# Optimization experiments

Measured on AMD Instinct MI355X. Metric: run time of the kernel, lower is better.

## Reference

```python
import jax, jax.numpy as jnp
import numpy as np

# Static multi-scale feature-map shapes (H, W) per level; sum(H*W) = 21760 = Len_in.
SPATIAL_SHAPES = ((128, 128), (64, 64), (32, 32), (16, 16))
N_HEADS, N_LEVELS, N_POINTS = 8, 4, 4


def _sample_level(v, loc, H, W):
    """Bilinear grid-sample, align_corners=False, zero padding.
    v:   (N, M, H*W, D) per-level value
    loc: (N, Lq, M, P, 2) sampling locations in [0,1] (x, y order)
    returns (N, Lq, M, P, D)
    """
    N, M, _, D = v.shape
    _, Lq, _, P, _ = loc.shape
    g = 2.0 * loc - 1.0                              # grid in [-1, 1]
    x = ((g[..., 0] + 1.0) * W - 1.0) * 0.5          # (N, Lq, M, P) pixel coords
    y = ((g[..., 1] + 1.0) * H - 1.0) * 0.5
    x0 = jnp.floor(x)
    y0 = jnp.floor(y)
    out = jnp.zeros((N, M, Lq * P, D), dtype=v.dtype)
    for dy in (0, 1):
        for dx in (0, 1):
            xi = x0 + dx
            yi = y0 + dy
            w = (1.0 - jnp.abs(x - xi)) * (1.0 - jnp.abs(y - yi))
            valid = (xi >= 0) & (xi <= W - 1) & (yi >= 0) & (yi <= H - 1)
            w = jnp.where(valid, w, 0.0)             # zero padding outside
            xc = jnp.clip(xi, 0, W - 1).astype(jnp.int32)
            yc = jnp.clip(yi, 0, H - 1).astype(jnp.int32)
            idx = yc * W + xc                        # (N, Lq, M, P)
            idx = jnp.transpose(idx, (0, 2, 1, 3)).reshape(N, M, Lq * P)
            gathered = jnp.take_along_axis(v, idx[..., None], axis=2)  # (N, M, Lq*P, D)
            wt = jnp.transpose(w, (0, 2, 1, 3)).reshape(N, M, Lq * P, 1)
            out = out + gathered * wt
    out = out.reshape(N, M, Lq, P, D)
    return jnp.transpose(out, (0, 2, 1, 3, 4))       # (N, Lq, M, P, D)


def _ms_deform_attn_core(value, sampling_locations, attention_weights):
    # value: (N, Len_in, M, D); locs: (N, Lq, M, L, P, 2); attn: (N, Lq, M, L, P)
    N, _, M, D = value.shape
    Lq = sampling_locations.shape[1]
    acc = jnp.zeros((N, Lq, M, D), dtype=value.dtype)
    start = 0
    for lid, (H, W) in enumerate(SPATIAL_SHAPES):
        v_l = value[:, start:start + H * W]                    # (N, H*W, M, D)
        v_l = jnp.transpose(v_l, (0, 2, 1, 3))                 # (N, M, H*W, D)
        samp = _sample_level(v_l, sampling_locations[:, :, :, lid], H, W)
        acc = acc + jnp.einsum('nqmpd,nqmp->nqmd', samp, attention_weights[:, :, :, lid])
        start += H * W
    return acc.reshape(N, Lq, M * D)


def setup_inputs() -> dict:
    key = jax.random.key(0)
    ks = jax.random.split(key, 12)
    N, Lq, C = 2, 21760, 256
    L, P, M = N_LEVELS, N_POINTS, N_HEADS
    s = 0.05  # keep logits / offsets in a sane range
    return {
        'query': jax.random.normal(ks[0], (N, Lq, C), jnp.float32),
        'reference_points': jax.random.uniform(ks[1], (N, Lq, L, 2), jnp.float32),
        'input_flatten': jax.random.normal(ks[2], (N, Lq, C), jnp.float32),
        'W_off': jax.random.normal(ks[3], (C, M * L * P * 2), jnp.float32) * s,
        'b_off': jax.random.normal(ks[4], (M * L * P * 2,), jnp.float32) * s,
        'W_attn': jax.random.normal(ks[5], (C, M * L * P), jnp.float32) * s,
        'b_attn': jax.random.normal(ks[6], (M * L * P,), jnp.float32) * s,
        'W_val': jax.random.normal(ks[7], (C, C), jnp.float32) * s,
        'b_val': jax.random.normal(ks[8], (C,), jnp.float32) * s,
        'W_out': jax.random.normal(ks[9], (C, C), jnp.float32) * s,
        'b_out': jax.random.normal(ks[10], (C,), jnp.float32) * s,
    }


def reference(query, reference_points, input_flatten, W_off, b_off,
              W_attn, b_attn, W_val, b_val, W_out, b_out):
    N, Lq, C = query.shape
    M, L, P = N_HEADS, N_LEVELS, N_POINTS
    D = C // M
    value = (input_flatten @ W_val + b_val).reshape(N, -1, M, D)
    offsets = (query @ W_off + b_off).reshape(N, Lq, M, L, P, 2)
    attn = (query @ W_attn + b_attn).reshape(N, Lq, M, L * P)
    attn = jax.nn.softmax(attn, axis=-1).reshape(N, Lq, M, L, P)
    # offset normalizer is (W_l, H_l) per level
    norm = jnp.array([[w, h] for (h, w) in SPATIAL_SHAPES], dtype=query.dtype)  # (L, 2)
    loc = (reference_points[:, :, None, :, None, :]
           + offsets / norm[None, None, None, :, None, :])   # (N, Lq, M, L, P, 2)
    out = _ms_deform_attn_core(value, loc, attn)
    return out @ W_out + b_out
```

## Files before the change

### kernel.cpp

```cpp
#include <hip/hip_runtime.h>

#define LQ     21760
#define NBATCH 2
#define MROWS  (NBATCH * LQ)
#define QB     (MROWS / 8)

typedef __attribute__((ext_vector_type(8))) short bf16x8;
typedef __attribute__((ext_vector_type(4))) float f32x4;

__device__ __forceinline__ unsigned short f2bf(float f) {
    unsigned u = __builtin_bit_cast(unsigned, f);
    return (unsigned short)((u + 0x7fffu + ((u >> 16) & 1u)) >> 16);
}
__device__ __forceinline__ float bf2f(unsigned short h) {
    return __builtin_bit_cast(float, (unsigned)h << 16);
}
__device__ __forceinline__ float f16lo(unsigned u) {
    return (float)__builtin_bit_cast(_Float16, (unsigned short)(u & 0xffffu));
}
__device__ __forceinline__ float f16hi(unsigned u) {
    return (float)__builtin_bit_cast(_Float16, (unsigned short)(u >> 16));
}

template <int CTRL>
__device__ __forceinline__ float fdpp(float v) {
    int r = __builtin_amdgcn_update_dpp(
        0, __builtin_bit_cast(int, v), CTRL, 0xf, 0xf, false);
    return __builtin_bit_cast(float, r);
}

__global__ __launch_bounds__(256) void cvt_wall(
    const float* __restrict__ Wv, const float* __restrict__ Wo,
    const float* __restrict__ Wa, const float* __restrict__ Wu,
    short* __restrict__ Wtv, short* __restrict__ Wcat, short* __restrict__ Wtu)
{
    int idx = blockIdx.x * 256 + threadIdx.x;
    if (idx < 65536) {
        int nn = idx >> 8, k = idx & 255;
        Wtv[idx] = (short)f2bf(Wv[k * 256 + nn]);
    } else if (idx < 131072) {
        int j = idx - 65536; int nn = j >> 8, k = j & 255;
        Wcat[j] = (short)f2bf(Wo[k * 256 + nn]);
    } else if (idx < 163840) {
        int j = idx - 131072; int nn = j >> 8, k = j & 255;
        Wcat[65536 + j] = (short)f2bf(Wa[k * 128 + nn]);
    } else if (idx < 229376) {
        int j = idx - 163840; int nn = j >> 8, k = j & 255;
        Wtu[j] = (short)f2bf(Wu[k * 256 + nn]);
    }
}

template <int AF32, int OMODE>
__global__ __launch_bounds__(256) void gemm_mfma(
    const void* __restrict__ Aptr,
    const short* __restrict__ Bt,
    const float* __restrict__ bias,
    const float* __restrict__ bias2,
    void* __restrict__ Cout,
    void* __restrict__ Cout2,
    int N)
{
    __shared__ short Al[128 * 64];
    __shared__ short Bl[128 * 64];

    const int tid  = threadIdx.x;
    const int lane = tid & 63, wid = tid >> 6;
    const int wr = wid >> 1, wc = wid & 1;
    const int bx = blockIdx.x, by = blockIdx.y;

    const long arow0 = (long)by * 128;
    const int  brow0 = bx * 128;

    const short* Abf = (const short*)Aptr;
    const float* Af  = (const float*)Aptr;

    f32x4 acc[4][4];
#pragma unroll
    for (int i = 0; i < 4; ++i)
#pragma unroll
        for (int j = 0; j < 4; ++j) acc[i][j] = (f32x4)0.f;

    bf16x8 ra[4], rb[4];
    float4 raf[4][2];

#pragma unroll
    for (int i = 0; i < 4; ++i) {
        int id = tid + i * 256, r = id >> 3, c = id & 7;
        if (AF32) {
            raf[i][0] = *(const float4*)(Af + (arow0 + r) * 256 + c * 8);
            raf[i][1] = *(const float4*)(Af + (arow0 + r) * 256 + c * 8 + 4);
        } else {
            ra[i] = *(const bf16x8*)(Abf + (arow0 + r) * 256 + c * 8);
        }
        rb[i] = *(const bf16x8*)(Bt + (long)(brow0 + r) * 256 + c * 8);
    }

    for (int step = 0; step < 4; ++step) {
#pragma unroll
        for (int i = 0; i < 4; ++i) {
            int id = tid + i * 256, r = id >> 3, c = id & 7;
            bf16x8 av;
            if (AF32) {
                unsigned q0, q1, q2, q3;
                asm("v_cvt_pk_bf16_f32 %0, %1, %2" : "=v"(q0) : "v"(raf[i][0].x), "v"(raf[i][0].y));
                asm("v_cvt_pk_bf16_f32 %0, %1, %2" : "=v"(q1) : "v"(raf[i][0].z), "v"(raf[i][0].w));
                asm("v_cvt_pk_bf16_f32 %0, %1, %2" : "=v"(q2) : "v"(raf[i][1].x), "v"(raf[i][1].y));
                asm("v_cvt_pk_bf16_f32 %0, %1, %2" : "=v"(q3) : "v"(raf[i][1].z), "v"(raf[i][1].w));
                uint4 u = make_uint4(q0, q1, q2, q3);
                av = __builtin_bit_cast(bf16x8, u);
            } else {
                av = ra[i];
            }
            *(bf16x8*)(Al + r * 64 + ((c ^ (r & 7)) * 8)) = av;
            *(bf16x8*)(Bl + r * 64 + ((c ^ (r & 7)) * 8)) = rb[i];
        }
        __syncthreads();
        if (step < 3) {
            const int k0 = (step + 1) * 64;
#pragma unroll
            for (int i = 0; i < 4; ++i) {
                int id = tid + i * 256, r = id >> 3, c = id & 7;
                if (AF32) {
                    raf[i][0] = *(const float4*)(Af + (arow0 + r) * 256 + k0 + c * 8);
                    raf[i][1] = *(const float4*)(Af + (arow0 + r) * 256 + k0 + c * 8 + 4);
                } else {
                    ra[i] = *(const bf16x8*)(Abf + (arow0 + r) * 256 + k0 + c * 8);
                }
                rb[i] = *(const bf16x8*)(Bt + (long)(brow0 + r) * 256 + k0 + c * 8);
            }
        }
#pragma unroll
        for (int kk = 0; kk < 2; ++kk) {
            const int g = lane >> 4;
            const int chunk = kk * 4 + g;
            bf16x8 af[4], bg[4];
#pragma unroll
            for (int mi = 0; mi < 4; ++mi) {
                int r = wr * 64 + mi * 16 + (lane & 15);
                af[mi] = *(const bf16x8*)(Al + r * 64 + ((chunk ^ (r & 7)) * 8));
            }
#pragma unroll
            for (int ni = 0; ni < 4; ++ni) {
                int r = wc * 64 + ni * 16 + (lane & 15);
                bg[ni] = *(const bf16x8*)(Bl + r * 64 + ((chunk ^ (r & 7)) * 8));
            }
#pragma unroll
            for (int mi = 0; mi < 4; ++mi)
#pragma unroll
                for (int ni = 0; ni < 4; ++ni)
                    acc[mi][ni] = __builtin_amdgcn_mfma_f32_16x16x32_bf16(
                        af[mi], bg[ni], acc[mi][ni], 0, 0, 0);
        }
        __syncthreads();
    }

#pragma unroll
    for (int mi = 0; mi < 4; ++mi) {
#pragma unroll
        for (int ni = 0; ni < 4; ++ni) {
            const int  col = bx * 128 + wc * 64 + ni * 16 + (lane & 15);
            const long row = (long)by * 128 + wr * 64 + mi * 16 + ((lane >> 4) * 4);
            float b;
            if (OMODE == 3) b = (col < 256) ? bias[col] : bias2[col - 256];
            else            b = bias[col];
#pragma unroll
            for (int q = 0; q < 4; ++q) {
                float v = acc[mi][ni][q] + b;
                if (OMODE == 0) {
                    ((float*)Cout)[(row + q) * N + col] = v;
                } else if (OMODE == 1) {
                    ((unsigned short*)Cout)[(row + q) * N + col] = f2bf(v);
                } else if (OMODE == 2) {
                    ((unsigned short*)Cout)[(row + q) * N + col] =
                        __builtin_bit_cast(unsigned short, (_Float16)v);
                } else if (OMODE == 4) {
                    const int mh = col >> 5, ch = col & 31;
                    ((unsigned short*)Cout)[((size_t)mh * MROWS + (row + q)) * 32 + ch] =
                        __builtin_bit_cast(unsigned short, (_Float16)v);
                } else {
                    if (col < 256) {
                        const int mh = col >> 5, ch = col & 31;
                        ((unsigned short*)Cout)[((size_t)mh * MROWS + (row + q)) * 32 + ch] = f2bf(v);
                    } else {
                        const int cc = col - 256;
                        const int mh = cc >> 4, k = cc & 15;
                        ((unsigned short*)Cout2)[((size_t)mh * MROWS + (row + q)) * 16 + k] = f2bf(v);
                    }
                }
            }
        }
    }
}

__global__ __launch_bounds__(256, 8) void ms_sample_f16v(
    const unsigned short* __restrict__ valuef16,
    const unsigned short* __restrict__ offbf,
    const unsigned short* __restrict__ attnbf,
    const float* __restrict__ refpts,
    unsigned short* __restrict__ accbf)
{
    __shared__ uint2 meta_lds[4][2][32];
    __shared__ float part[4][2][32][10];

    const int lane = threadIdx.x & 63;
    const int wid  = threadIdx.x >> 6;
    const int b    = blockIdx.x;
    const int m    = b / QB;
    const int qblk = b - m * QB;
    const int qn0w = qblk * 8 + 2 * wid;

    const int p   = lane & 15;
    const int cy  = (lane >> 4) & 1;
    const int th  = lane >> 5;
    const int lvl = p >> 2;
    const int pt  = p & 3;
    const int qnl = qn0w + th;
    const int nb  = (qnl >= LQ) ? 1 : 0;

    const size_t hq = (size_t)m * MROWS + qnl;

    float lg = bf2f(attnbf[hq * 16 + p]);

    float mx = lg;
    mx = fmaxf(mx, fdpp<0x128>(mx));
    mx = fmaxf(mx, fdpp<0x124>(mx));
    mx = fmaxf(mx, fdpp<0x122>(mx));
    mx = fmaxf(mx, fdpp<0x121>(mx));
    float e = __expf(lg - mx);
    float s = e;
    s += fdpp<0x128>(s);
    s += fdpp<0x124>(s);
    s += fdpp<0x122>(s);
    s += fdpp<0x121>(s);
    const float aw = e * (1.0f / s);

    const int W  = 128 >> lvl;
    const int st = (lvl == 0) ? 0 : (lvl == 1) ? 16384
                 : (lvl == 2) ? 20480 : 21504;
    const float fW = (float)W;

    const float2 rxy = *(const float2*)&refpts[(size_t)qnl * 8 + lvl * 2];
    unsigned oo = *(const unsigned*)(offbf + hq * 32 + lvl * 8 + pt * 2);
    const float ox = bf2f((unsigned short)(oo & 0xffff));
    const float oy = bf2f((unsigned short)(oo >> 16));

    const float x = fmaf(rxy.x, fW, ox) - 0.5f;
    const float y = fmaf(rxy.y, fW, oy) - 0.5f;
    const float x0f = floorf(x), y0f = floorf(y);
    const float fx = x - x0f, fy = y - y0f;
    const int x0i = (int)x0f;
    const int yi  = (int)y0f + cy;

    const bool yok = (yi >= 0) & (yi <= W - 1);
    const float awwy = yok ? aw * (cy ? fy : (1.0f - fy)) : 0.0f;
    const int yc = min(max(yi, 0), W - 1);

    const bool x0ok = (x0i >= 0) & (x0i <= W - 1);
    const bool x1ok = (x0i + 1 >= 0) & (x0i + 1 <= W - 1);
    const float w0f = x0ok ? awwy * (1.0f - fx) : 0.0f;
    const float w1f = x1ok ? awwy * fx : 0.0f;

    const int bxp = min(max(x0i, 0), W - 2);
    const bool base_is_x0 = (x0i == bxp);
    const float wl = base_is_x0 ? w0f : w1f;
    const float wr = base_is_x0 ? w1f : w0f;
    const int addr = nb * 21760 + st + yc * W + bxp;

    const unsigned wp =
        (unsigned)__builtin_bit_cast(unsigned short, (_Float16)wl) |
        ((unsigned)__builtin_bit_cast(unsigned short, (_Float16)wr) << 16);
    meta_lds[wid][th][p * 2 + cy] = make_uint2((unsigned)addr, wp);

    asm volatile("s_waitcnt lgkmcnt(0)" ::: "memory");
    __builtin_amdgcn_sched_barrier(0);

    const int cg   = lane & 7;
    const int slot = lane >> 3;
    const char* vbh = (const char*)(valuef16 + (size_t)m * MROWS * 32);
    const unsigned mc = (unsigned)(cg * 16);
    const int wsh = (cg >> 2) << 4;

    float a0[8] = {}, a1[8] = {};
#pragma unroll
    for (int t = 0; t < 2; ++t) {
        uint2 mt[4];
#pragma unroll
        for (int it = 0; it < 4; ++it)
            mt[it] = meta_lds[wid][t][it * 8 + slot];

        uint4 vv[4];
#pragma unroll
        for (int it = 0; it < 4; ++it)
            vv[it] = *(const uint4*)(vbh + (((size_t)mt[it].x) << 6) + mc);

        float* a = t ? a1 : a0;
#pragma unroll
        for (int it = 0; it < 4; ++it) {
            const float w = (float)__builtin_bit_cast(
                _Float16, (unsigned short)((mt[it].y >> wsh) & 0xffffu));
            a[0] = fmaf(f16lo(vv[it].x), w, a[0]);
            a[1] = fmaf(f16hi(vv[it].x), w, a[1]);
            a[2] = fmaf(f16lo(vv[it].y), w, a[2]);
            a[3] = fmaf(f16hi(vv[it].y), w, a[3]);
            a[4] = fmaf(f16lo(vv[it].z), w, a[4]);
            a[5] = fmaf(f16hi(vv[it].z), w, a[5]);
            a[6] = fmaf(f16lo(vv[it].w), w, a[6]);
            a[7] = fmaf(f16hi(vv[it].w), w, a[7]);
        }
    }

#pragma unroll
    for (int jj = 0; jj < 8; ++jj) { a0[jj] += fdpp<0x128>(a0[jj]); a1[jj] += fdpp<0x128>(a1[jj]); }

    if ((lane & 8) == 0) {
        const int idx = (lane >> 4) * 8 + cg;
        float* pp0 = &part[wid][0][idx][0];
        float* pp1 = &part[wid][1][idx][0];
        *(float2*)&pp0[0] = make_float2(a0[0], a0[1]);
        *(float2*)&pp0[2] = make_float2(a0[2], a0[3]);
        *(float2*)&pp0[4] = make_float2(a0[4], a0[5]);
        *(float2*)&pp0[6] = make_float2(a0[6], a0[7]);
        *(float2*)&pp1[0] = make_float2(a1[0], a1[1]);
        *(float2*)&pp1[2] = make_float2(a1[2], a1[3]);
        *(float2*)&pp1[4] = make_float2(a1[4], a1[5]);
        *(float2*)&pp1[6] = make_float2(a1[6], a1[7]);
    }
    asm volatile("s_waitcnt lgkmcnt(0)" ::: "memory");
    __builtin_amdgcn_sched_barrier(0);

    {
        const int t  = lane >> 5;
        const int ch = lane & 31;
        const int o  = ch >> 3, k = ch & 7;
        float sum = 0.f;
#pragma unroll
        for (int grp = 0; grp < 4; ++grp)
            sum += part[wid][t][grp * 8 + o][k] + part[wid][t][grp * 8 + o + 4][k];
        accbf[(size_t)(qn0w + t) * 256 + m * 32 + ch] = f2bf(sum);
    }
}

__global__ __launch_bounds__(256) void gemm_k256(
    const float* __restrict__ A, const float* __restrict__ B,
    const float* __restrict__ bias, float* __restrict__ C,
    int M, int N)
{
    __shared__ float As[16][68];
    __shared__ float Bs[16][68];

    const int tid = threadIdx.x;
    const int tx = tid & 15, ty = tid >> 4;
    const int bx = blockIdx.x, by = blockIdx.y;

    const int arow = tid >> 2;
    const int ak   = (tid & 3) << 2;
    const int bk   = tid >> 4;
    const int bcol = (tid & 15) << 2;

    const float* Ag = A + (long)(by * 64 + arow) * 256 + ak;
    const float* Bg = B + (long)bk * N + bx * 64 + bcol;

    float acc[4][4] = {};

    for (int k0 = 0; k0 < 256; k0 += 16) {
        float4 av = *(const float4*)(Ag + k0);
        float4 bv = *(const float4*)(Bg + (long)k0 * N);
        As[ak + 0][arow] = av.x;
        As[ak + 1][arow] = av.y;
        As[ak + 2][arow] = av.z;
        As[ak + 3][arow] = av.w;
        *(float4*)&Bs[bk][bcol] = bv;
        __syncthreads();
#pragma unroll
        for (int k = 0; k < 16; ++k) {
            float4 a4 = *(const float4*)&As[k][ty * 4];
            float4 b4 = *(const float4*)&Bs[k][tx * 4];
            float a[4] = {a4.x, a4.y, a4.z, a4.w};
            float bb[4] = {b4.x, b4.y, b4.z, b4.w};
#pragma unroll
            for (int i = 0; i < 4; ++i)
#pragma unroll
                for (int j = 0; j < 4; ++j)
                    acc[i][j] = fmaf(a[i], bb[j], acc[i][j]);
        }
        __syncthreads();
    }

    float4 b4 = *(const float4*)&bias[bx * 64 + tx * 4];
#pragma unroll
    for (int i = 0; i < 4; ++i) {
        float4 o;
        o.x = acc[i][0] + b4.x;
        o.y = acc[i][1] + b4.y;
        o.z = acc[i][2] + b4.z;
        o.w = acc[i][3] + b4.w;
        *(float4*)&C[(long)(by * 64 + ty * 4 + i) * N + bx * 64 + tx * 4] = o;
    }
}

__global__ __launch_bounds__(256) void ms_sample_f32(
    const float* __restrict__ value,
    const float* __restrict__ offraw,
    const float* __restrict__ attnraw,
    const float* __restrict__ refpts,
    float* __restrict__ acc_out)
{
    const int lane = threadIdx.x & 63;
    const int wid  = threadIdx.x >> 6;
    const long t   = (long)blockIdx.x * 4 + wid;

    const int  m  = (int)(t & 7);
    const long qn = t >> 3;

    const int p   = lane >> 2;
    const int c   = lane & 3;
    const int cx  = c & 1, cy = c >> 1;
    const int lvl = p >> 2;
    const int pt  = p & 3;

    float lg = attnraw[qn * 128 + m * 16 + p];
    float mx = lg;
    mx = fmaxf(mx, __shfl_xor(mx, 4));
    mx = fmaxf(mx, __shfl_xor(mx, 8));
    mx = fmaxf(mx, __shfl_xor(mx, 16));
    mx = fmaxf(mx, __shfl_xor(mx, 32));
    float e = __expf(lg - mx);
    float s = e;
    s += __shfl_xor(s, 4);
    s += __shfl_xor(s, 8);
    s += __shfl_xor(s, 16);
    s += __shfl_xor(s, 32);
    const float aw = e * (1.0f / s);

    const int W  = 128 >> lvl;
    const int st = (lvl == 0) ? 0 : (lvl == 1) ? 16384
                 : (lvl == 2) ? 20480 : 21504;
    const float fW = (float)W;

    const float2 rxy = *(const float2*)&refpts[qn * 8 + lvl * 2];
    float2 o2 = *(const float2*)(offraw + qn * 256 + m * 32 + lvl * 8 + pt * 2);

    const float x = fmaf(rxy.x, fW, o2.x) - 0.5f;
    const float y = fmaf(rxy.y, fW, o2.y) - 0.5f;
    const float x0f = floorf(x), y0f = floorf(y);
    const float fx = x - x0f, fy = y - y0f;
    const int xi = (int)x0f + cx;
    const int yi = (int)y0f + cy;
    const float wx = cx ? fx : (1.0f - fx);
    const float wy = cy ? fy : (1.0f - fy);
    const bool ok = (xi >= 0) & (xi <= W - 1) & (yi >= 0) & (yi <= W - 1);
    const float wt = ok ? aw * wx * wy : 0.0f;
    const int xc = min(max(xi, 0), W - 1);
    const int yc = min(max(yi, 0), W - 1);
    const int addr = st + yc * W + xc;

    const int cg   = lane & 7;
    const int slot = lane >> 3;

    const long nn = qn / LQ;
    const float4* v4 = (const float4*)(value + (nn * (long)LQ) * 256 + m * 32);

    float4 acc = make_float4(0.f, 0.f, 0.f, 0.f);
#pragma unroll
    for (int it = 0; it < 8; ++it) {
        const int src = 8 * it + slot;
        const int   a = __shfl(addr, src);
        const float w = __shfl(wt, src);
        const float4 v = v4[(long)a * 64 + cg];
        acc.x = fmaf(w, v.x, acc.x);
        acc.y = fmaf(w, v.y, acc.y);
        acc.z = fmaf(w, v.z, acc.z);
        acc.w = fmaf(w, v.w, acc.w);
    }

#pragma unroll
    for (int mask = 8; mask <= 32; mask <<= 1) {
        acc.x += __shfl_xor(acc.x, mask);
        acc.y += __shfl_xor(acc.y, mask);
        acc.z += __shfl_xor(acc.z, mask);
        acc.w += __shfl_xor(acc.w, mask);
    }

    if (lane < 8)
        *(float4*)(acc_out + qn * 256 + m * 32 + cg * 4) = acc;
}

__global__ __launch_bounds__(256) void outproj_inplace(
    float* __restrict__ io, const float* __restrict__ W,
    const float* __restrict__ bias)
{
    __shared__ float As[32][260];
    __shared__ float Bs[16][260];

    const int tid = threadIdx.x;
    const long rbase = (long)blockIdx.x * 32;

#pragma unroll
    for (int i = 0; i < 8; ++i) {
        int f4 = i * 256 + tid;
        int r  = f4 >> 6;
        int c4 = (f4 & 63) << 2;
        float4 v = *(const float4*)&io[(rbase + r) * 256 + c4];
        *(float4*)&As[r][c4] = v;
    }
    __syncthreads();

    const int tx = tid & 15, ty = tid >> 4;
    float acc[2][16] = {};

    for (int k0 = 0; k0 < 256; k0 += 16) {
#pragma unroll
        for (int i = 0; i < 4; ++i) {
            int f4 = i * 256 + tid;
            int kr = f4 >> 6;
            int c4 = (f4 & 63) << 2;
            float4 v = *(const float4*)&W[(long)(k0 + kr) * 256 + c4];
            *(float4*)&Bs[kr][c4] = v;
        }
        __syncthreads();
#pragma unroll
        for (int k = 0; k < 16; ++k) {
            float a0 = As[ty * 2 + 0][k0 + k];
            float a1 = As[ty * 2 + 1][k0 + k];
#pragma unroll
            for (int jj = 0; jj < 4; ++jj) {
                float4 b = *(const float4*)&Bs[k][tx * 4 + jj * 64];
                acc[0][jj * 4 + 0] = fmaf(a0, b.x, acc[0][jj * 4 + 0]);
                acc[0][jj * 4 + 1] = fmaf(a0, b.y, acc[0][jj * 4 + 1]);
                acc[0][jj * 4 + 2] = fmaf(a0, b.z, acc[0][jj * 4 + 2]);
                acc[0][jj * 4 + 3] = fmaf(a0, b.w, acc[0][jj * 4 + 3]);
                acc[1][jj * 4 + 0] = fmaf(a1, b.x, acc[1][jj * 4 + 0]);
                acc[1][jj * 4 + 1] = fmaf(a1, b.y, acc[1][jj * 4 + 1]);
                acc[1][jj * 4 + 2] = fmaf(a1, b.z, acc[1][jj * 4 + 2]);
                acc[1][jj * 4 + 3] = fmaf(a1, b.w, acc[1][jj * 4 + 3]);
            }
        }
        __syncthreads();
    }

#pragma unroll
    for (int i = 0; i < 2; ++i)
#pragma unroll
        for (int jj = 0; jj < 4; ++jj) {
            float4 b = *(const float4*)&bias[tx * 4 + jj * 64];
            float4 o;
            o.x = acc[i][jj * 4 + 0] + b.x;
            o.y = acc[i][jj * 4 + 1] + b.y;
            o.z = acc[i][jj * 4 + 2] + b.z;
            o.w = acc[i][jj * 4 + 3] + b.w;
            *(float4*)&io[(rbase + ty * 2 + i) * 256 + tx * 4 + jj * 64] = o;
        }
}

extern "C" void kernel_launch(void* const* d_in, const int* in_sizes, int n_in,
                              void* d_out, int out_size, void* d_ws, size_t ws_size,
                              hipStream_t stream)
{
    const float* query         = (const float*)d_in[0];
    const float* refpts        = (const float*)d_in[1];
    const float* input_flatten = (const float*)d_in[2];
    const float* W_off         = (const float*)d_in[3];
    const float* b_off         = (const float*)d_in[4];
    const float* W_attn        = (const float*)d_in[5];
    const float* b_attn        = (const float*)d_in[6];
    const float* W_val         = (const float*)d_in[7];
    const float* b_val         = (const float*)d_in[8];
    const float* W_out         = (const float*)d_in[9];
    const float* b_out         = (const float*)d_in[10];
    float* out = (float*)d_out;

    dim3 blk(256);

    const size_t NEED_BF = 78446592ULL;
    if (ws_size >= NEED_BF) {
        char* w = (char*)d_ws;
        unsigned short* valuef16 = (unsigned short*)w;
        unsigned short* offbf    = (unsigned short*)(w + 22282240);
        unsigned short* attnbf   = (unsigned short*)(w + 44564480);
        unsigned short* accbf    = (unsigned short*)(w + 55705600);
        short*          Wtv      = (short*)(w + 77987840);
        short*          Wcat     = (short*)(w + 78118912);
        short*          Wtu      = (short*)(w + 78315520);

        cvt_wall<<<dim3(896), blk, 0, stream>>>(
            W_val, W_off, W_attn, W_out, Wtv, Wcat, Wtu);

        gemm_mfma<1, 4><<<dim3(2, MROWS / 128), blk, 0, stream>>>(
            input_flatten, Wtv, b_val, nullptr, valuef16, nullptr, 256);
        gemm_mfma<1, 3><<<dim3(3, MROWS / 128), blk, 0, stream>>>(
            query, Wcat, b_off, b_attn, offbf, attnbf, 384);

        ms_sample_f16v<<<dim3(MROWS / 8 * 8), blk, 0, stream>>>(
            valuef16, offbf, attnbf, refpts, accbf);

        gemm_mfma<0, 0><<<dim3(2, MROWS / 128), blk, 0, stream>>>(
            accbf, Wtu, b_out, nullptr, out, nullptr, 256);
    } else {
        float* ws = (float*)d_ws;
        float* value   = ws;
        float* offraw  = value  + (long)MROWS * 256;
        float* attnraw = offraw + (long)MROWS * 256;
        float* accbuf  = attnraw + (long)MROWS * 128;

        const size_t need_with_acc =
            ((size_t)MROWS * 256 * 3 + (size_t)MROWS * 128) * sizeof(float);
        const bool has_acc = ws_size >= need_with_acc;

        gemm_k256<<<dim3(4, MROWS / 64), blk, 0, stream>>>(input_flatten, W_val, b_val, value, MROWS, 256);
        gemm_k256<<<dim3(4, MROWS / 64), blk, 0, stream>>>(query, W_off, b_off, offraw, MROWS, 256);
        gemm_k256<<<dim3(2, MROWS / 64), blk, 0, stream>>>(query, W_attn, b_attn, attnraw, MROWS, 128);

        float* accp = has_acc ? accbuf : out;
        ms_sample_f32<<<dim3((NBATCH * LQ * 8) / 4), blk, 0, stream>>>(
            value, offraw, attnraw, refpts, accp);

        if (has_acc)
            gemm_k256<<<dim3(4, MROWS / 64), blk, 0, stream>>>(accbuf, W_out, b_out, out, MROWS, 256);
        else
            outproj_inplace<<<dim3(MROWS / 32), blk, 0, stream>>>(out, W_out, b_out);
    }
}
```

Baseline: 159.3 us.

## Process four queries per wave in deformable sampling kernel

Each wave of the sampling kernel now handles four queries instead of two. Each lane computes both y-corner rows for its point instead of splitting rows across lanes, so the per-query setup (softmax, coordinate math, offset/ref loads) is shared across more gathers. The grid shrinks by half and each wave issues four batches of gathers back to back for more memory-level parallelism. In exchange it needs more registers and LDS per block, and the occupancy hint drops from 8 to 7 blocks per CU.

```diff
diff --git a/kernel.cpp b/kernel.cpp
--- a/kernel.cpp
+++ b/kernel.cpp
@@ -3,7 +3,7 @@
 #define LQ     21760
 #define NBATCH 2
 #define MROWS  (NBATCH * LQ)
-#define QB     (MROWS / 8)
+#define QB16   (MROWS / 16)
 
 typedef __attribute__((ext_vector_type(8))) short bf16x8;
 typedef __attribute__((ext_vector_type(4))) float f32x4;
@@ -192,29 +192,39 @@
     }
 }
 
-__global__ __launch_bounds__(256, 8) void ms_sample_f16v(
+__device__ __forceinline__ void fma8(float (&a)[8], uint4 v, float w) {
+    a[0] = fmaf(f16lo(v.x), w, a[0]);
+    a[1] = fmaf(f16hi(v.x), w, a[1]);
+    a[2] = fmaf(f16lo(v.y), w, a[2]);
+    a[3] = fmaf(f16hi(v.y), w, a[3]);
+    a[4] = fmaf(f16lo(v.z), w, a[4]);
+    a[5] = fmaf(f16hi(v.z), w, a[5]);
+    a[6] = fmaf(f16lo(v.w), w, a[6]);
+    a[7] = fmaf(f16hi(v.w), w, a[7]);
+}
+
+__global__ __launch_bounds__(256, 7) void ms_sample_f16v(
     const unsigned short* __restrict__ valuef16,
     const unsigned short* __restrict__ offbf,
     const unsigned short* __restrict__ attnbf,
     const float* __restrict__ refpts,
     unsigned short* __restrict__ accbf)
 {
-    __shared__ uint2 meta_lds[4][2][32];
-    __shared__ float part[4][2][32][10];
+    __shared__ uint2 meta_lds[4][4][32];
+    __shared__ float part[4][4][32][10];
 
     const int lane = threadIdx.x & 63;
     const int wid  = threadIdx.x >> 6;
     const int b    = blockIdx.x;
-    const int m    = b / QB;
-    const int qblk = b - m * QB;
-    const int qn0w = qblk * 8 + 2 * wid;
+    const int m    = b / QB16;
+    const int qblk = b - m * QB16;
+    const int qn0w = qblk * 16 + 4 * wid;
 
     const int p   = lane & 15;
-    const int cy  = (lane >> 4) & 1;
-    const int th  = lane >> 5;
+    const int tq  = lane >> 4;
     const int lvl = p >> 2;
     const int pt  = p & 3;
-    const int qnl = qn0w + th;
+    const int qnl = qn0w + tq;
     const int nb  = (qnl >= LQ) ? 1 : 0;
 
     const size_t hq = (size_t)m * MROWS + qnl;
@@ -249,27 +259,37 @@
     const float x0f = floorf(x), y0f = floorf(y);
     const float fx = x - x0f, fy = y - y0f;
     const int x0i = (int)x0f;
-    const int yi  = (int)y0f + cy;
-
-    const bool yok = (yi >= 0) & (yi <= W - 1);
-    const float awwy = yok ? aw * (cy ? fy : (1.0f - fy)) : 0.0f;
-    const int yc = min(max(yi, 0), W - 1);
+    const int y0i = (int)y0f;
+
+    const bool y0ok = (y0i >= 0) & (y0i <= W - 1);
+    const bool y1ok = (y0i + 1 >= 0) & (y0i + 1 <= W - 1);
+    const float awwy0 = y0ok ? aw * (1.0f - fy) : 0.0f;
+    const float awwy1 = y1ok ? aw * fy : 0.0f;
+    const int yc0 = min(max(y0i, 0), W - 1);
+    const int yc1 = min(max(y0i + 1, 0), W - 1);
 
     const bool x0ok = (x0i >= 0) & (x0i <= W - 1);
     const bool x1ok = (x0i + 1 >= 0) & (x0i + 1 <= W - 1);
-    const float w0f = x0ok ? awwy * (1.0f - fx) : 0.0f;
-    const float w1f = x1ok ? awwy * fx : 0.0f;
-
+    const float wx0 = x0ok ? (1.0f - fx) : 0.0f;
+    const float wx1 = x1ok ? fx : 0.0f;
     const int bxp = min(max(x0i, 0), W - 2);
-    const bool base_is_x0 = (x0i == bxp);
-    const float wl = base_is_x0 ? w0f : w1f;
-    const float wr = base_is_x0 ? w1f : w0f;
-    const int addr = nb * 21760 + st + yc * W + bxp;
-
-    const unsigned wp =
-        (unsigned)__builtin_bit_cast(unsigned short, (_Float16)wl) |
-        ((unsigned)__builtin_bit_cast(unsigned short, (_Float16)wr) << 16);
-    meta_lds[wid][th][p * 2 + cy] = make_uint2((unsigned)addr, wp);
+    const bool bis = (x0i == bxp);
+    const float wxl = bis ? wx0 : wx1;
+    const float wxr = bis ? wx1 : wx0;
+
+    const int base0 = nb * 21760 + st + bxp;
+    const int addr0 = base0 + yc0 * W;
+    const int addr1 = base0 + yc1 * W;
+
+    const unsigned wp0 =
+        (unsigned)__builtin_bit_cast(unsigned short, (_Float16)(awwy0 * wxl)) |
+        ((unsigned)__builtin_bit_cast(unsigned short, (_Float16)(awwy0 * wxr)) << 16);
+    const unsigned wp1 =
+        (unsigned)__builtin_bit_cast(unsigned short, (_Float16)(awwy1 * wxl)) |
+        ((unsigned)__builtin_bit_cast(unsigned short, (_Float16)(awwy1 * wxr)) << 16);
+
+    meta_lds[wid][tq][p * 2 + 0] = make_uint2((unsigned)addr0, wp0);
+    meta_lds[wid][tq][p * 2 + 1] = make_uint2((unsigned)addr1, wp1);
 
     asm volatile("s_waitcnt lgkmcnt(0)" ::: "memory");
     __builtin_amdgcn_sched_barrier(0);
@@ -280,42 +300,43 @@
     const unsigned mc = (unsigned)(cg * 16);
     const int wsh = (cg >> 2) << 4;
 
-    float a0[8] = {}, a1[8] = {};
-#pragma unroll
-    for (int t = 0; t < 2; ++t) {
+    float a0[8] = {}, a1[8] = {}, a2[8] = {}, a3[8] = {};
+
+    auto do_task = [&](int t, float (&a)[8]) {
         uint2 mt[4];
 #pragma unroll
         for (int it = 0; it < 4; ++it)
             mt[it] = meta_lds[wid][t][it * 8 + slot];
-
         uint4 vv[4];
 #pragma unroll
         for (int it = 0; it < 4; ++it)
             vv[it] = *(const uint4*)(vbh + (((size_t)mt[it].x) << 6) + mc);
-
-        float* a = t ? a1 : a0;
 #pragma unroll
         for (int it = 0; it < 4; ++it) {
             const float w = (float)__builtin_bit_cast(
                 _Float16, (unsigned short)((mt[it].y >> wsh) & 0xffffu));
-            a[0] = fmaf(f16lo(vv[it].x), w, a[0]);
-            a[1] = fmaf(f16hi(vv[it].x), w, a[1]);
-            a[2] = fmaf(f16lo(vv[it].y), w, a[2]);
-            a[3] = fmaf(f16hi(vv[it].y), w, a[3]);
-            a[4] = fmaf(f16lo(vv[it].z), w, a[4]);
-            a[5] = fmaf(f16hi(vv[it].z), w, a[5]);
-            a[6] = fmaf(f16lo(vv[it].w), w, a[6]);
-            a[7] = fmaf(f16hi(vv[it].w), w, a[7]);
-        }
-    }
-
-#pragma unroll
-    for (int jj = 0; jj < 8; ++jj) { a0[jj] += fdpp<0x128>(a0[jj]); a1[jj] += fdpp<0x128>(a1[jj]); }
+            fma8(a, vv[it], w);
+        }
+    };
+    do_task(0, a0);
+    do_task(1, a1);
+    do_task(2, a2);
+    do_task(3, a3);
+
+#pragma unroll
+    for (int jj = 0; jj < 8; ++jj) {
+        a0[jj] += fdpp<0x128>(a0[jj]);
+        a1[jj] += fdpp<0x128>(a1[jj]);
+        a2[jj] += fdpp<0x128>(a2[jj]);
+        a3[jj] += fdpp<0x128>(a3[jj]);
+    }
 
     if ((lane & 8) == 0) {
         const int idx = (lane >> 4) * 8 + cg;
         float* pp0 = &part[wid][0][idx][0];
         float* pp1 = &part[wid][1][idx][0];
+        float* pp2 = &part[wid][2][idx][0];
+        float* pp3 = &part[wid][3][idx][0];
         *(float2*)&pp0[0] = make_float2(a0[0], a0[1]);
         *(float2*)&pp0[2] = make_float2(a0[2], a0[3]);
         *(float2*)&pp0[4] = make_float2(a0[4], a0[5]);
@@ -324,12 +345,21 @@
         *(float2*)&pp1[2] = make_float2(a1[2], a1[3]);
         *(float2*)&pp1[4] = make_float2(a1[4], a1[5]);
         *(float2*)&pp1[6] = make_float2(a1[6], a1[7]);
+        *(float2*)&pp2[0] = make_float2(a2[0], a2[1]);
+        *(float2*)&pp2[2] = make_float2(a2[2], a2[3]);
+        *(float2*)&pp2[4] = make_float2(a2[4], a2[5]);
+        *(float2*)&pp2[6] = make_float2(a2[6], a2[7]);
+        *(float2*)&pp3[0] = make_float2(a3[0], a3[1]);
+        *(float2*)&pp3[2] = make_float2(a3[2], a3[3]);
+        *(float2*)&pp3[4] = make_float2(a3[4], a3[5]);
+        *(float2*)&pp3[6] = make_float2(a3[6], a3[7]);
     }
     asm volatile("s_waitcnt lgkmcnt(0)" ::: "memory");
     __builtin_amdgcn_sched_barrier(0);
 
-    {
-        const int t  = lane >> 5;
+#pragma unroll
+    for (int tt = 0; tt < 2; ++tt) {
+        const int t  = (lane >> 5) * 2 + tt;
         const int ch = lane & 31;
         const int o  = ch >> 3, k = ch & 7;
         float sum = 0.f;
@@ -590,7 +620,7 @@
         gemm_mfma<1, 3><<<dim3(3, MROWS / 128), blk, 0, stream>>>(
             query, Wcat, b_off, b_attn, offbf, attnbf, 384);
 
-        ms_sample_f16v<<<dim3(MROWS / 8 * 8), blk, 0, stream>>>(
+        ms_sample_f16v<<<dim3(QB16 * 8), blk, 0, stream>>>(
             valuef16, offbf, attnbf, refpts, accbf);
 
         gemm_mfma<0, 0><<<dim3(2, MROWS / 128), blk, 0, stream>>>(
```

After: 151.2 us (median of 2 runs). 5.1% less time.
